# Optimization experiments

Measured on AMD Instinct MI355X. Metric: run time of the kernel, lower is better.

Reference implementation:

```python
import jax, jax.numpy as jnp
import numpy as np

N = 8192       # tokens
D = 1024       # input_dim
H = 1024       # hidden_dim
E = 8          # num_experts
K = 2          # top-k


def setup_inputs() -> dict:
    key = jax.random.key(0)
    ks = jax.random.split(key, 7)
    s_in = 1.0 / np.sqrt(D)
    s_h = 1.0 / np.sqrt(H)
    return {
        "x": jax.random.normal(ks[0], (N, D), dtype=jnp.float32),
        "W1": jax.random.uniform(ks[1], (E, D, H), jnp.float32, -s_in, s_in),
        "b1": jax.random.uniform(ks[2], (E, H), jnp.float32, -s_in, s_in),
        "W2": jax.random.uniform(ks[3], (E, H, H), jnp.float32, -s_h, s_h),
        "b2": jax.random.uniform(ks[4], (E, H), jnp.float32, -s_h, s_h),
        "Wg": jax.random.uniform(ks[5], (E, D), jnp.float32, -s_in, s_in),
        "bg": jax.random.uniform(ks[6], (E,), jnp.float32, -s_in, s_in),
    }


def reference(x, W1, b1, W2, b2, Wg, bg):
    # Gate: logits [N, E] -> top-k values/indices -> softmax over the k values
    logits = x @ Wg.T + bg
    topk_vals, topk_idx = jax.lax.top_k(logits, K)          # [N, K]
    gates = jax.nn.softmax(topk_vals, axis=1)               # [N, K]

    # Experts (dropout is identity in eval): two Linear+ReLU per expert
    h1 = jax.nn.relu(jnp.einsum('nd,edh->neh', x, W1) + b1[None])   # [N, E, H]
    h2 = jax.nn.relu(jnp.einsum('neh,ehf->nef', h1, W2) + b2[None]) # [N, E, H]

    # Gather each token's top-k expert outputs and combine with gate weights
    sel = jnp.take_along_axis(h2, topk_idx[:, :, None], axis=1)     # [N, K, H]
    return jnp.sum(gates[:, :, None] * sel, axis=1)                  # [N, H]
```

## Files before the change

### kernel.cpp

```cpp
#include <hip/hip_runtime.h>
#include <stdint.h>

#define N_TOK   8192
#define DIMK    1024
#define NEXP    8
#define PADROWS 17408

typedef __attribute__((ext_vector_type(8))) short short8;
typedef __attribute__((ext_vector_type(4))) float f32x4;
typedef unsigned short u16;

__device__ __forceinline__ u16 f2bf(float f) {
  uint32_t u = __builtin_bit_cast(uint32_t, f);
  u += 0x7fffu + ((u >> 16) & 1u);
  return (u16)(u >> 16);
}

__device__ __forceinline__ void load16_lds(const void* g, void* l) {
  __builtin_amdgcn_global_load_lds(
      (const __attribute__((address_space(1))) void*)g,
      (__attribute__((address_space(3))) void*)l, 16, 0, 0);
}

#define OFF_W1T   0u
#define OFF_W2T   16777216u
#define OFF_XP    33554432u
#define OFF_H1    69206016u
#define OFF_GIDX  104857600u
#define OFF_GVAL  104923136u
#define OFF_PTOK  104988672u
#define OFF_PGATE 105058304u
#define OFF_CTRL  105127936u

__global__ void convw_kernel(const float* __restrict__ W1, const float* __restrict__ W2,
                             u16* __restrict__ W1T, u16* __restrict__ W2T) {
  int idx = (int)blockIdx.x * 256 + (int)threadIdx.x;
  const float* src = W1; u16* dst = W1T;
  const int half = NEXP * 1024 * 64;
  if (idx >= half) { src = W2; dst = W2T; idx -= half; }
  const int k = idx & 1023;
  const int rest = idx >> 10;
  const int n0 = (rest & 63) << 4;
  const int e = rest >> 6;
  const float* s = src + ((size_t)e << 20) + ((size_t)k << 10) + n0;
  u16* d = dst + ((size_t)e << 20) + ((size_t)n0 << 10) + k;
#pragma unroll
  for (int i = 0; i < 16; ++i) d[(size_t)i << 10] = f2bf(s[i]);
}

__global__ void gate_kernel(const float* __restrict__ x, const float* __restrict__ Wg,
                            const float* __restrict__ bg, int* __restrict__ gidx,
                            float* __restrict__ gval, int* __restrict__ counts) {
  __shared__ int hist[NEXP];
  const int tid = (int)threadIdx.x;
  if (tid < NEXP) hist[tid] = 0;
  __syncthreads();
  const int n = (int)blockIdx.x * 4 + (tid >> 6);
  const int lane = tid & 63;
  float acc[NEXP];
#pragma unroll
  for (int e = 0; e < NEXP; ++e) acc[e] = 0.f;
  const float4* xr = (const float4*)(x + ((size_t)n << 10));
#pragma unroll
  for (int j = 0; j < 4; ++j) {
    float4 xv = xr[j * 64 + lane];
#pragma unroll
    for (int e = 0; e < NEXP; ++e) {
      float4 wv = ((const float4*)(Wg + ((size_t)e << 10)))[j * 64 + lane];
      acc[e] += xv.x * wv.x + xv.y * wv.y + xv.z * wv.z + xv.w * wv.w;
    }
  }
#pragma unroll
  for (int e = 0; e < NEXP; ++e)
#pragma unroll
    for (int off = 32; off; off >>= 1) acc[e] += __shfl_xor(acc[e], off, 64);
  if (lane == 0) {
    float lg[NEXP];
#pragma unroll
    for (int e = 0; e < NEXP; ++e) lg[e] = acc[e] + bg[e];
    int e0 = 0; float v0 = lg[0];
#pragma unroll
    for (int e = 1; e < NEXP; ++e) if (lg[e] > v0) { v0 = lg[e]; e0 = e; }
    int e1 = -1; float v1 = -1e30f;
#pragma unroll
    for (int e = 0; e < NEXP; ++e) if (e != e0 && lg[e] > v1) { v1 = lg[e]; e1 = e; }
    float t = expf(v1 - v0);
    float g0 = 1.f / (1.f + t);
    gidx[2 * n] = e0; gidx[2 * n + 1] = e1;
    gval[2 * n] = g0; gval[2 * n + 1] = t * g0;
    atomicAdd(&hist[e0], 1); atomicAdd(&hist[e1], 1);
  }
  __syncthreads();
  if (tid < NEXP && hist[tid]) atomicAdd(&counts[tid], hist[tid]);
}

__global__ void scan_kernel(const int* __restrict__ counts, int* __restrict__ poff) {
  if (threadIdx.x == 0) {
    int off = 0; poff[0] = 0;
    for (int e = 0; e < NEXP; ++e) { off += ((counts[e] + 127) >> 7) << 7; poff[e + 1] = off; }
  }
}

__global__ void scatter_kernel(const int* __restrict__ gidx, const float* __restrict__ gval,
                               const int* __restrict__ poff, int* __restrict__ cursor,
                               int* __restrict__ ptok, float* __restrict__ pgate) {
  const int n = (int)blockIdx.x * 256 + (int)threadIdx.x;
#pragma unroll
  for (int k = 0; k < 2; ++k) {
    const int e = gidx[2 * n + k];
    const int p = poff[e] + atomicAdd(&cursor[e], 1);
    ptok[p] = n;
    pgate[p] = gval[2 * n + k];
  }
}

__global__ void gather_kernel(const float* __restrict__ x, const int* __restrict__ ptok,
                              u16* __restrict__ xp) {
  const int p = (int)blockIdx.x * 4 + ((int)threadIdx.x >> 6);
  const int lane = (int)threadIdx.x & 63;
  const int tok = ptok[p];
  const float4* src = (const float4*)(x + ((size_t)tok << 10));
  ushort4* dst = (ushort4*)(xp + ((size_t)p << 10));
#pragma unroll
  for (int j = 0; j < 4; ++j) {
    float4 v = src[j * 64 + lane];
    ushort4 o; o.x = f2bf(v.x); o.y = f2bf(v.y); o.z = f2bf(v.z); o.w = f2bf(v.w);
    dst[j * 64 + lane] = o;
  }
}

template <int PASS>
__global__ __launch_bounds__(256, 2)
void gemm_kernel(const u16* __restrict__ A, const u16* __restrict__ WT,
                 const float* __restrict__ bias, const int* __restrict__ poff,
                 const int* __restrict__ ptok, const float* __restrict__ pgate,
                 u16* __restrict__ Hout, float* __restrict__ Out,
                 int* __restrict__ qhead) {
  __shared__ u16 As[2][128 * 64];
  __shared__ u16 Bs[2][128 * 64];
  __shared__ int tokS[128];
  __shared__ float gateS[128];
  __shared__ int tileS;

  const int tid = (int)threadIdx.x;
  const int lane = tid & 63;
  const int wid = tid >> 6;
  const int wm = (wid >> 1) * 64;
  const int wn = (wid & 1) * 64;
  const int r_in = lane >> 3;
  const int s_phys = lane & 7;

  const int total = (poff[NEXP] >> 7) * 8;

  for (;;) {
    if (tid == 0) tileS = atomicAdd(qhead, 1);
    __syncthreads();
    const int tile = tileS;
    if (tile >= total) break;
    const int rt = tile >> 3;
    const int ct = tile & 7;
    const int row0 = rt * 128;
    int e = 0;
    while (row0 >= poff[e + 1]) ++e;

    const u16* Ab = A + ((size_t)row0 << 10);
    const u16* Bb = WT + ((size_t)e << 20) + ((size_t)(ct * 128) << 10);

    if (PASS == 2 && tid < 128) {
      tokS[tid] = ptok[row0 + tid];
      gateS[tid] = pgate[row0 + tid];
    }

    f32x4 acc[4][4] = {};

#define STAGE(BUF, K0)                                                         \
  {                                                                            \
    _Pragma("unroll")                                                          \
    for (int i = 0; i < 4; ++i) {                                              \
      const int chunk = wid * 4 + i;                                           \
      const int row = chunk * 8 + r_in;                                        \
      const int slotL = s_phys ^ (row & 7);                                    \
      const size_t goff = ((size_t)row << 10) + (size_t)((K0) + slotL * 8);    \
      load16_lds(Ab + goff, &As[BUF][chunk * 512]);                            \
      load16_lds(Bb + goff, &Bs[BUF][chunk * 512]);                            \
    }                                                                          \
  }

#define COMPUTE(BUF)                                                           \
  {                                                                            \
    _Pragma("unroll")                                                          \
    for (int kk = 0; kk < 2; ++kk) {                                           \
      short8 af[4], bf_[4];                                                    \
      const int kslot = kk * 4 + (lane >> 4);                                  \
      _Pragma("unroll")                                                        \
      for (int mi = 0; mi < 4; ++mi) {                                         \
        const int m = wm + mi * 16 + (lane & 15);                              \
        af[mi] = *(const short8*)((const char*)&As[BUF][0] + m * 128 +         \
                                  ((kslot ^ (m & 7)) << 4));                   \
      }                                                                        \
      _Pragma("unroll")                                                        \
      for (int ni = 0; ni < 4; ++ni) {                                         \
        const int n = wn + ni * 16 + (lane & 15);                              \
        bf_[ni] = *(const short8*)((const char*)&Bs[BUF][0] + n * 128 +        \
                                   ((kslot ^ (n & 7)) << 4));                  \
      }                                                                        \
      _Pragma("unroll")                                                        \
      for (int mi = 0; mi < 4; ++mi)                                           \
        _Pragma("unroll")                                                      \
        for (int ni = 0; ni < 4; ++ni)                                         \
          acc[mi][ni] = __builtin_amdgcn_mfma_f32_16x16x32_bf16(               \
              af[mi], bf_[ni], acc[mi][ni], 0, 0, 0);                          \
    }                                                                          \
  }

    STAGE(0, 0)
    __syncthreads();
    int cur = 0;
#pragma unroll 1
    for (int t = 0; t < 15; ++t) {
      const int nb = cur ^ 1;
      STAGE(nb, (t + 1) * 64)
      COMPUTE(cur)
      __syncthreads();
      cur = nb;
    }
    COMPUTE(cur)

    const float* bb = bias + (e << 10) + ct * 128;
    const int cbase = lane & 15;
    const int rbase = (lane >> 4) * 4;
#pragma unroll
    for (int ni = 0; ni < 4; ++ni) {
      const int col = wn + ni * 16 + cbase;
      const float bv = bb[col];
#pragma unroll
      for (int mi = 0; mi < 4; ++mi) {
        const int mb = wm + mi * 16 + rbase;
#pragma unroll
        for (int j = 0; j < 4; ++j) {
          float v = fmaxf(acc[mi][ni][j] + bv, 0.0f);
          if (PASS == 1) {
            Hout[((size_t)(row0 + mb + j) << 10) + (size_t)(ct * 128 + col)] = f2bf(v);
          } else {
            const int m = mb + j;
            unsafeAtomicAdd(Out + ((size_t)tokS[m] << 10) + (size_t)(ct * 128 + col),
                            v * gateS[m]);
          }
        }
      }
    }
#undef STAGE
#undef COMPUTE
  }
}

extern "C" void kernel_launch(void* const* d_in, const int* in_sizes, int n_in,
                              void* d_out, int out_size, void* d_ws, size_t ws_size,
                              hipStream_t stream) {
  (void)in_sizes; (void)n_in; (void)ws_size;
  const float* x  = (const float*)d_in[0];
  const float* W1 = (const float*)d_in[1];
  const float* b1 = (const float*)d_in[2];
  const float* W2 = (const float*)d_in[3];
  const float* b2 = (const float*)d_in[4];
  const float* Wg = (const float*)d_in[5];
  const float* bg = (const float*)d_in[6];
  float* out = (float*)d_out;
  char* ws = (char*)d_ws;

  u16*   W1T   = (u16*)(ws + OFF_W1T);
  u16*   W2T   = (u16*)(ws + OFF_W2T);
  u16*   xp    = (u16*)(ws + OFF_XP);
  u16*   h1    = (u16*)(ws + OFF_H1);
  int*   gidx  = (int*)(ws + OFF_GIDX);
  float* gval  = (float*)(ws + OFF_GVAL);
  int*   ptok  = (int*)(ws + OFF_PTOK);
  float* pgate = (float*)(ws + OFF_PGATE);
  int*   counts = (int*)(ws + OFF_CTRL);
  int*   cursor = counts + 8;
  int*   poff   = counts + 16;
  int*   qh1    = counts + 25;
  int*   qh2    = counts + 26;

  hipMemsetAsync(d_out, 0, (size_t)out_size * 4, stream);
  hipMemsetAsync(ws + OFF_PTOK, 0, 139392, stream);

  convw_kernel<<<4096, 256, 0, stream>>>(W1, W2, W1T, W2T);
  gate_kernel<<<N_TOK / 4, 256, 0, stream>>>(x, Wg, bg, gidx, gval, counts);
  scan_kernel<<<1, 64, 0, stream>>>(counts, poff);
  scatter_kernel<<<N_TOK / 256, 256, 0, stream>>>(gidx, gval, poff, cursor, ptok, pgate);
  gather_kernel<<<PADROWS / 4, 256, 0, stream>>>(x, ptok, xp);
  gemm_kernel<1><<<512, 256, 0, stream>>>(xp, W1T, b1, poff, ptok, pgate, h1, nullptr, qh1);
  gemm_kernel<2><<<512, 256, 0, stream>>>(h1, W2T, b2, poff, ptok, pgate, nullptr, out, qh2);
}
```

Before: 344.6 us.

## Tile weight transpose through LDS and pipeline GEMM loads with partial vmcnt waits

The weight conversion kernel now transposes 64x64 tiles through shared memory, so both its global reads and writes are coalesced and vectorized instead of strided 2-byte scattered stores. The expert GEMM main loop is fully unrolled and the __syncthreads pairs are replaced with explicit s_waitcnt vmcnt(8)/lgkmcnt(0) plus raw barriers. This lets the next stage's global-to-LDS loads stay in flight while only the current buffer's loads are awaited. The hand-written wait counts depend on the exact number of outstanding loads per STAGE and are fragile.

Result: faster. 323.7 us (-6.0%).

```diff
diff --git a/kernel.cpp b/kernel.cpp
--- a/kernel.cpp
+++ b/kernel.cpp
@@ -34,18 +34,39 @@
 
 __global__ void convw_kernel(const float* __restrict__ W1, const float* __restrict__ W2,
                              u16* __restrict__ W1T, u16* __restrict__ W2T) {
-  int idx = (int)blockIdx.x * 256 + (int)threadIdx.x;
+  __shared__ u16 tile[64][65];
+  int b = (int)blockIdx.x;
   const float* src = W1; u16* dst = W1T;
-  const int half = NEXP * 1024 * 64;
-  if (idx >= half) { src = W2; dst = W2T; idx -= half; }
-  const int k = idx & 1023;
-  const int rest = idx >> 10;
-  const int n0 = (rest & 63) << 4;
-  const int e = rest >> 6;
-  const float* s = src + ((size_t)e << 20) + ((size_t)k << 10) + n0;
-  u16* d = dst + ((size_t)e << 20) + ((size_t)n0 << 10) + k;
-#pragma unroll
-  for (int i = 0; i < 16; ++i) d[(size_t)i << 10] = f2bf(s[i]);
+  if (b >= 2048) { src = W2; dst = W2T; b -= 2048; }
+  const int e  = b >> 8;
+  const int t  = b & 255;
+  const int k0 = (t >> 4) << 6;
+  const int n0 = (t & 15) << 6;
+  const int tid = (int)threadIdx.x;
+  const int r  = tid >> 2;
+  const int c4 = (tid & 3) << 4;
+  const float4* s = (const float4*)(src + ((size_t)e << 20) +
+                                    ((size_t)(k0 + r) << 10) + n0 + c4);
+#pragma unroll
+  for (int j = 0; j < 4; ++j) {
+    float4 v = s[j];
+    tile[r][c4 + 4 * j + 0] = f2bf(v.x);
+    tile[r][c4 + 4 * j + 1] = f2bf(v.y);
+    tile[r][c4 + 4 * j + 2] = f2bf(v.z);
+    tile[r][c4 + 4 * j + 3] = f2bf(v.w);
+  }
+  __syncthreads();
+  const int on = tid >> 2;
+  const int ok = (tid & 3) << 4;
+  u16* d = dst + ((size_t)e << 20) + ((size_t)(n0 + on) << 10) + k0 + ok;
+  short8 v0, v1;
+#pragma unroll
+  for (int j = 0; j < 8; ++j) {
+    v0[j] = (short)tile[ok + j][on];
+    v1[j] = (short)tile[ok + 8 + j][on];
+  }
+  *(short8*)d = v0;
+  *(short8*)(d + 8) = v1;
 }
 
 __global__ void gate_kernel(const float* __restrict__ x, const float* __restrict__ Wg,
@@ -214,17 +235,19 @@
   }
 
     STAGE(0, 0)
-    __syncthreads();
-    int cur = 0;
-#pragma unroll 1
-    for (int t = 0; t < 15; ++t) {
-      const int nb = cur ^ 1;
-      STAGE(nb, (t + 1) * 64)
-      COMPUTE(cur)
-      __syncthreads();
-      cur = nb;
+#pragma unroll
+    for (int t = 0; t < 16; ++t) {
+      if (t < 15) {
+        STAGE((t + 1) & 1, (t + 1) * 64)
+        asm volatile("s_waitcnt vmcnt(8)" ::: "memory");
+      } else {
+        asm volatile("s_waitcnt vmcnt(0)" ::: "memory");
+      }
+      __builtin_amdgcn_s_barrier();
+      COMPUTE(t & 1)
+      asm volatile("s_waitcnt lgkmcnt(0)" ::: "memory");
+      __builtin_amdgcn_s_barrier();
     }
-    COMPUTE(cur)
 
     const float* bb = bias + (e << 10) + ct * 128;
     const int cbase = lane & 15;
```
